# Optimization experiments

Measured on AMD Instinct MI355X. Metric: run time of the kernel, lower is better.

The kernel has to match this reference:

```python
import jax, jax.numpy as jnp
import numpy as np

B, SX, SY, D = 32, 2048, 2048, 160

def setup_inputs() -> dict:
    key = jax.random.key(0)
    ks = jax.random.split(key, 5)
    s = 1.0 / np.sqrt(D)
    return {
        "x": jax.random.normal(ks[0], (B, SX, D), dtype=jnp.float32),
        "y": jax.random.normal(ks[1], (B, SY, D), dtype=jnp.float32),
        "Wq": jax.random.normal(ks[2], (D, D), dtype=jnp.float32) * s,
        "bq": jnp.zeros((D,), dtype=jnp.float32),
        "Wk": jax.random.normal(ks[3], (D, D), dtype=jnp.float32) * s,
        "bk": jnp.zeros((D,), dtype=jnp.float32),
        "Wv": jax.random.normal(ks[4], (D, D), dtype=jnp.float32) * s,
        "bv": jnp.zeros((D,), dtype=jnp.float32),
    }

def reference(x, y, Wq, bq, Wk, bk, Wv, bv):
    # torch nn.Linear: out = in @ W.T + b, W is [out_dim, in_dim]
    q = jnp.einsum('bxd,ed->bxe', x, Wq) + bq          # [B,SX,D]
    k = jnp.einsum('byd,ed->bye', y, Wk) + bk          # [B,SY,D]
    v = jnp.einsum('byd,ed->bye', y, Wv) + bv          # [B,SY,D]
    scores = jnp.einsum('bxd,byd->bxy', q, k)          # [B,SX,SY] (no scaling in source)
    attn = jax.nn.softmax(scores, axis=-1)
    out = jnp.einsum('bxy,byd->bxd', attn, v)          # dropout is identity at eval
    return out + x                                     # residual
```

## Files before the change

kernel.cpp:

```cpp
#include <hip/hip_runtime.h>

#define LOG2E 1.44269504088896340736f

typedef _Float16 f16;
typedef __attribute__((ext_vector_type(2))) _Float16 f16x2;
typedef __attribute__((ext_vector_type(4))) _Float16 f16x4;
typedef __attribute__((ext_vector_type(8))) _Float16 f16x8;
typedef __attribute__((ext_vector_type(4))) float f32x4;
typedef __attribute__((ext_vector_type(16))) float f32x16;
typedef __attribute__((ext_vector_type(8))) unsigned short us8;

#define BB 32
#define SSX 2048
#define SSY 2048
#define DD 160
#define M_TOTAL (BB*SSX)

#define PRS 168
#define VTRS 136
#define RS 168

__device__ __forceinline__ f32x4 mfma16(f16x8 a, f16x8 b, f32x4 c) {
  return __builtin_amdgcn_mfma_f32_16x16x32_f16(a, b, c, 0, 0, 0);
}

__device__ __forceinline__ f32x16 mfma32(f16x8 a, f16x8 b, f32x16 c) {
  return __builtin_amdgcn_mfma_f32_32x32x16_f16(a, b, c, 0, 0, 0);
}

__device__ __forceinline__ unsigned pk2(float a, float b) {
  union { f16x2 h; unsigned u; } x;
  x.h = (f16x2){(f16)a, (f16)b};
  return x.u;
}

__global__ __launch_bounds__(256, 3) void proj_kernel(
    const float* __restrict__ x, const float* __restrict__ y,
    const float* __restrict__ Wq, const float* __restrict__ bq,
    const float* __restrict__ Wk, const float* __restrict__ bk,
    const float* __restrict__ Wv, const float* __restrict__ bv,
    f16* __restrict__ Qw, f16* __restrict__ Kw, f16* __restrict__ Vtw)
{
  __shared__ __align__(16) f16 buf[160*PRS];
  const int t = threadIdx.x;
  const int wave = t >> 6;
  const int lane = t & 63;
  const int quad = lane >> 4;
  const int l16  = lane & 15;
  const int bid  = (blockIdx.x & 7) * 192 + (blockIdx.x >> 3);
  const int kind = bid % 3;
  const int tile = bid / 3;
  const int row0 = tile * 128;
  const float* src  = (kind == 0) ? x  : y;
  const float* W    = (kind == 0) ? Wq : (kind == 1 ? Wk : Wv);
  const float* bias = (kind == 0) ? bq : (kind == 1 ? bk : bv);

  for (int i = 0; i < 20; ++i) {
    int idx = t + i*256;
    int r = idx / 40, c4 = idx % 40;
    float4 v = *(const float4*)&src[(size_t)(row0 + r)*DD + c4*4];
    f16x4 h = { (f16)v.x, (f16)v.y, (f16)v.z, (f16)v.w };
    *(f16x4*)&buf[r*PRS + c4*4] = h;
  }
  __syncthreads();
  f16x8 afr0[5], afr1[5];
  #pragma unroll
  for (int ks = 0; ks < 5; ++ks) {
    afr0[ks] = *(const f16x8*)&buf[(wave*32 + l16)*PRS + ks*32 + quad*8];
    afr1[ks] = *(const f16x8*)&buf[(wave*32 + 16 + l16)*PRS + ks*32 + quad*8];
  }
  __syncthreads();

  for (int i = 0; i < 25; ++i) {
    int idx = t + i*256;
    int r = idx / 40, c4 = idx % 40;
    float4 v = *(const float4*)&W[r*160 + c4*4];
    f16x4 h = { (f16)v.x, (f16)v.y, (f16)v.z, (f16)v.w };
    *(f16x4*)&buf[r*PRS + c4*4] = h;
  }
  __syncthreads();

  f32x4 acc0[10], acc1[10];
  #pragma unroll
  for (int nt = 0; nt < 10; ++nt) {
    float bs = bias[nt*16 + l16];
    acc0[nt] = (f32x4){bs,bs,bs,bs};
    acc1[nt] = (f32x4){bs,bs,bs,bs};
    #pragma unroll
    for (int ks = 0; ks < 5; ++ks) {
      f16x8 bfr = *(const f16x8*)&buf[(nt*16 + l16)*PRS + ks*32 + quad*8];
      acc0[nt] = mfma16(afr0[ks], bfr, acc0[nt]);
      acc1[nt] = mfma16(afr1[ks], bfr, acc1[nt]);
    }
  }
  __syncthreads();

  if (kind < 2) {
    f16* dst = (kind == 0) ? Qw : Kw;
    #pragma unroll
    for (int nt = 0; nt < 10; ++nt)
      #pragma unroll
      for (int r = 0; r < 4; ++r) {
        buf[(wave*32 + quad*4 + r)*PRS + nt*16 + l16]      = (f16)acc0[nt][r];
        buf[(wave*32 + 16 + quad*4 + r)*PRS + nt*16 + l16] = (f16)acc1[nt][r];
      }
    __syncthreads();
    for (int i = 0; i < 10; ++i) {
      int idx = t + i*256;
      int r = idx / 20, g = idx % 20;
      *(us8*)&dst[(size_t)(row0 + r)*DD + g*8] = *(const us8*)&buf[r*PRS + g*8];
    }
  } else {
    #pragma unroll
    for (int nt = 0; nt < 10; ++nt)
      #pragma unroll
      for (int r = 0; r < 4; ++r) {
        buf[(nt*16 + l16)*VTRS + wave*32 + quad*4 + r]      = (f16)acc0[nt][r];
        buf[(nt*16 + l16)*VTRS + wave*32 + 16 + quad*4 + r] = (f16)acc1[nt][r];
      }
    __syncthreads();
    const int b  = row0 / SSY;
    const int y0 = row0 % SSY;
    for (int i = 0; i < 10; ++i) {
      int idx = t + i*256;
      int d = idx / 16, yg = idx % 16;
      *(us8*)&Vtw[((size_t)b*DD + d)*SSY + y0 + yg*8] = *(const us8*)&buf[d*VTRS + yg*8];
    }
  }
}


#define LOAD_CHUNK(yb) { \
  const f16* ksrc = Kw + ((size_t)b*SSY + (yb))*DD; \
  const f16* vsrc = Vtw + (size_t)b*DD*SSY + (yb); \
  _Pragma("unroll") \
  for (int i = 0; i < 5; ++i) { \
    int idx = t + i*256; int r = idx/20, c = idx%20; \
    kreg[i] = *(const us8*)&ksrc[(size_t)r*DD + c*8]; \
  } \
  _Pragma("unroll") \
  for (int i = 0; i < 5; ++i) { \
    int idx = t + i*256; int d = idx>>3, g = idx&7; \
    vreg[i] = *(const us8*)&vsrc[(size_t)d*SSY + g*8]; \
  } \
}

#define STORE_CHUNK() { \
  _Pragma("unroll") \
  for (int i = 0; i < 5; ++i) { \
    int idx = t + i*256; int r = idx/20, c = idx%20; \
    *(us8*)&K_lds[r*RS + c*8] = kreg[i]; \
  } \
  _Pragma("unroll") \
  for (int i = 0; i < 5; ++i) { \
    int idx = t + i*256; int d = idx>>3, g = idx&7; \
    *(us8*)&Vt_lds[d*64 + ((g ^ (d & 7)) << 3)] = vreg[i]; \
  } \
}

__global__ __launch_bounds__(256, 2) void flash_kernel(
    const f16* __restrict__ Qw, const f16* __restrict__ Kw, const f16* __restrict__ Vtw,
    const float* __restrict__ x, float* __restrict__ out)
{
  __shared__ __align__(16) f16 K_lds[64*RS];
  __shared__ __align__(16) f16 Vt_lds[160*64];
  const int t = threadIdx.x;
  const int wave = t >> 6;
  const int lane = t & 63;
  const int l31  = lane & 31;
  const int hi   = lane >> 5;
  const int bid  = (blockIdx.x & 7) * 64 + (blockIdx.x >> 3);
  const int b    = bid >> 4;
  const int x0   = (bid & 15) * 128;

  us8 kreg[5], vreg[5];
  LOAD_CHUNK(0);

  f16x8 qfr[10];
  #pragma unroll
  for (int h = 0; h < 2; ++h) {
    if (h) __syncthreads();
    const f16* qsrc = Qw + ((size_t)b*SSX + x0 + h*64)*DD;
    for (int i = 0; i < 5; ++i) {
      int idx = t + i*256;
      int r = idx / 20, c = idx % 20;
      *(us8*)&K_lds[r*RS + c*8] = *(const us8*)&qsrc[(size_t)r*DD + c*8];
    }
    __syncthreads();
    if ((wave >> 1) == h) {
      const int base = (wave & 1)*32;
      #pragma unroll
      for (int s = 0; s < 10; ++s)
        qfr[s] = *(const f16x8*)&K_lds[(base + l31)*RS + s*16 + hi*8];
    }
  }

  f32x16 acc[5];
  #pragma unroll
  for (int i = 0; i < 5; ++i)
    #pragma unroll
    for (int r = 0; r < 16; ++r) acc[i][r] = 0.f;
  float m = -1e30f, l = 0.f;

  for (int yc = 0; yc < SSY/64; ++yc) {
    __syncthreads();
    STORE_CHUNK();
    __syncthreads();
    if (yc < SSY/64 - 1) LOAD_CHUNK((yc+1)*64);

    f32x16 S0, S1;
    #pragma unroll
    for (int r = 0; r < 16; ++r) { S0[r] = 0.f; S1[r] = 0.f; }
    __builtin_amdgcn_s_setprio(1);
    #pragma unroll
    for (int s = 0; s < 10; ++s) {
      f16x8 k0 = *(const f16x8*)&K_lds[l31*RS + s*16 + hi*8];
      f16x8 k1 = *(const f16x8*)&K_lds[(32 + l31)*RS + s*16 + hi*8];
      S0 = mfma32(k0, qfr[s], S0);
      S1 = mfma32(k1, qfr[s], S1);
    }
    __builtin_amdgcn_s_setprio(0);

    float pmax = fmaxf(S0[0], S0[1]);
    #pragma unroll
    for (int r = 2; r < 16; r += 2) pmax = fmaxf(pmax, fmaxf(S0[r], S0[r+1]));
    #pragma unroll
    for (int r = 0; r < 16; r += 2) pmax = fmaxf(pmax, fmaxf(S1[r], S1[r+1]));
    pmax = fmaxf(pmax, __shfl_xor(pmax, 32));

    if (__any(pmax > m + 8.f)) {
      float n  = fmaxf(m, pmax);
      float sc = exp2f((m - n)*LOG2E);
      m = n; l *= sc;
      #pragma unroll
      for (int r = 0; r < 16; ++r) {
        float scq = __shfl(sc, (r&3) + 8*(r>>2) + 4*hi);
        #pragma unroll
        for (int dt = 0; dt < 5; ++dt) acc[dt][r] *= scq;
      }
    }

    float lsum = 0.f;
    #pragma unroll
    for (int r = 0; r < 16; ++r) { S0[r] = exp2f((S0[r] - m)*LOG2E); lsum += S0[r]; }
    #pragma unroll
    for (int r = 0; r < 16; ++r) { S1[r] = exp2f((S1[r] - m)*LOG2E); lsum += S1[r]; }
    lsum += __shfl_xor(lsum, 32);
    l += lsum;

    #pragma unroll
    for (int c = 0; c < 4; ++c) {
      const int bo = (c & 1)*8;
      unsigned L0, L1, H0, H1;
      if (c < 2) {
        L0 = pk2(S0[bo+0], S0[bo+1]); L1 = pk2(S0[bo+2], S0[bo+3]);
        H0 = pk2(S0[bo+4], S0[bo+5]); H1 = pk2(S0[bo+6], S0[bo+7]);
      } else {
        L0 = pk2(S1[bo+0], S1[bo+1]); L1 = pk2(S1[bo+2], S1[bo+3]);
        H0 = pk2(S1[bo+4], S1[bo+5]); H1 = pk2(S1[bo+6], S1[bo+7]);
      }
      unsigned sd0 = hi ? L0 : H0;
      unsigned sd1 = hi ? L1 : H1;
      unsigned rc0 = (unsigned)__shfl_xor((int)sd0, 32);
      unsigned rc1 = (unsigned)__shfl_xor((int)sd1, 32);
      union { unsigned u[4]; f16x8 h; } pw;
      pw.u[0] = hi ? rc0 : L0;
      pw.u[1] = hi ? rc1 : L1;
      pw.u[2] = hi ? H0 : rc0;
      pw.u[3] = hi ? H1 : rc1;
      __builtin_amdgcn_s_setprio(1);
      #pragma unroll
      for (int dt = 0; dt < 5; ++dt) {
        int row = dt*32 + l31;
        f16x8 vf = *(const f16x8*)&Vt_lds[row*64 + (((c*2 + hi) ^ (row & 7)) << 3)];
        acc[dt] = mfma32(pw.h, vf, acc[dt]);
      }
      __builtin_amdgcn_s_setprio(0);
    }
  }

  #pragma unroll
  for (int r = 0; r < 16; ++r) {
    int qr = (r&3) + 8*(r>>2) + 4*hi;
    float rl = 1.f / __shfl(l, qr);
    size_t rowoff = ((size_t)b*SSX + x0 + wave*32 + qr)*DD + l31;
    #pragma unroll
    for (int dt = 0; dt < 5; ++dt) {
      size_t o = rowoff + (size_t)dt*32;
      out[o] = acc[dt][r]*rl + x[o];
    }
  }
}

extern "C" void kernel_launch(void* const* d_in, const int* in_sizes, int n_in,
                              void* d_out, int out_size, void* d_ws, size_t ws_size,
                              hipStream_t stream) {
  const float* x  = (const float*)d_in[0];
  const float* y  = (const float*)d_in[1];
  const float* Wq = (const float*)d_in[2];
  const float* bq = (const float*)d_in[3];
  const float* Wk = (const float*)d_in[4];
  const float* bk = (const float*)d_in[5];
  const float* Wv = (const float*)d_in[6];
  const float* bv = (const float*)d_in[7];

  f16* Qw  = (f16*)d_ws;
  f16* Kw  = Qw + (size_t)M_TOTAL*DD;
  f16* Vtw = Kw + (size_t)M_TOTAL*DD;

  proj_kernel<<<1536, 256, 0, stream>>>(x, y, Wq, bq, Wk, bk, Wv, bv, Qw, Kw, Vtw);
  flash_kernel<<<512, 256, 0, stream>>>(Qw, Kw, Vtw, x, (float*)d_out);
}
```

Measured before the change: 282.0 us.

## Read V fragments straight from global, double-buffer K in LDS, use permlane32 swap

V^T is no longer staged through LDS. Each wave loads its MFMA B-operand fragments for V directly from global memory into registers, split into two halves so the loads can overlap with the softmax work. K is double-buffered in LDS, which removes one of the two barriers per iteration. The P repacking now uses round-toward-zero pack conversion and permlane32_swap in place of two shuffles plus selects. The cost is more global and L2 traffic, because every wave reads the full V tile, plus higher register pressure from holding 20 V fragments, which risks occupancy and exposed global latency.

New measurement: 417.0 us. 47.9% more time.

```diff
diff --git a/kernel.cpp b/kernel.cpp
--- a/kernel.cpp
+++ b/kernel.cpp
@@ -4,11 +4,13 @@
 
 typedef _Float16 f16;
 typedef __attribute__((ext_vector_type(2))) _Float16 f16x2;
+typedef __attribute__((ext_vector_type(2))) __fp16 fp16x2;
 typedef __attribute__((ext_vector_type(4))) _Float16 f16x4;
 typedef __attribute__((ext_vector_type(8))) _Float16 f16x8;
 typedef __attribute__((ext_vector_type(4))) float f32x4;
 typedef __attribute__((ext_vector_type(16))) float f32x16;
 typedef __attribute__((ext_vector_type(8))) unsigned short us8;
+typedef __attribute__((ext_vector_type(2))) int i32x2;
 
 #define BB 32
 #define SSX 2048
@@ -28,9 +30,9 @@
   return __builtin_amdgcn_mfma_f32_32x32x16_f16(a, b, c, 0, 0, 0);
 }
 
-__device__ __forceinline__ unsigned pk2(float a, float b) {
-  union { f16x2 h; unsigned u; } x;
-  x.h = (f16x2){(f16)a, (f16)b};
+__device__ __forceinline__ unsigned pk2rtz(float a, float b) {
+  union { fp16x2 h; unsigned u; } x;
+  x.h = __builtin_amdgcn_cvt_pkrtz(a, b);
   return x.u;
 }
 
@@ -130,31 +132,20 @@
 }
 
 
-#define LOAD_CHUNK(yb) { \
+#define LOAD_K(yb) { \
   const f16* ksrc = Kw + ((size_t)b*SSY + (yb))*DD; \
-  const f16* vsrc = Vtw + (size_t)b*DD*SSY + (yb); \
   _Pragma("unroll") \
   for (int i = 0; i < 5; ++i) { \
     int idx = t + i*256; int r = idx/20, c = idx%20; \
     kreg[i] = *(const us8*)&ksrc[(size_t)r*DD + c*8]; \
   } \
-  _Pragma("unroll") \
-  for (int i = 0; i < 5; ++i) { \
-    int idx = t + i*256; int d = idx>>3, g = idx&7; \
-    vreg[i] = *(const us8*)&vsrc[(size_t)d*SSY + g*8]; \
-  } \
-}
-
-#define STORE_CHUNK() { \
+}
+
+#define STORE_K(cb) { \
   _Pragma("unroll") \
   for (int i = 0; i < 5; ++i) { \
     int idx = t + i*256; int r = idx/20, c = idx%20; \
-    *(us8*)&K_lds[r*RS + c*8] = kreg[i]; \
-  } \
-  _Pragma("unroll") \
-  for (int i = 0; i < 5; ++i) { \
-    int idx = t + i*256; int d = idx>>3, g = idx&7; \
-    *(us8*)&Vt_lds[d*64 + ((g ^ (d & 7)) << 3)] = vreg[i]; \
+    *(us8*)&K_lds[cb][r*RS + c*8] = kreg[i]; \
   } \
 }
 
@@ -162,8 +153,7 @@
     const f16* __restrict__ Qw, const f16* __restrict__ Kw, const f16* __restrict__ Vtw,
     const float* __restrict__ x, float* __restrict__ out)
 {
-  __shared__ __align__(16) f16 K_lds[64*RS];
-  __shared__ __align__(16) f16 Vt_lds[160*64];
+  __shared__ __align__(16) f16 K_lds[2][64*RS];
   const int t = threadIdx.x;
   const int wave = t >> 6;
   const int lane = t & 63;
@@ -173,27 +163,38 @@
   const int b    = bid >> 4;
   const int x0   = (bid & 15) * 128;
 
-  us8 kreg[5], vreg[5];
-  LOAD_CHUNK(0);
+  us8 kreg[5];
+  LOAD_K(0);
 
   f16x8 qfr[10];
-  #pragma unroll
-  for (int h = 0; h < 2; ++h) {
-    if (h) __syncthreads();
-    const f16* qsrc = Qw + ((size_t)b*SSX + x0 + h*64)*DD;
-    for (int i = 0; i < 5; ++i) {
-      int idx = t + i*256;
-      int r = idx / 20, c = idx % 20;
-      *(us8*)&K_lds[r*RS + c*8] = *(const us8*)&qsrc[(size_t)r*DD + c*8];
-    }
-    __syncthreads();
-    if ((wave >> 1) == h) {
-      const int base = (wave & 1)*32;
-      #pragma unroll
-      for (int s = 0; s < 10; ++s)
-        qfr[s] = *(const f16x8*)&K_lds[(base + l31)*RS + s*16 + hi*8];
-    }
-  }
+  const f16* qsrc = Qw + ((size_t)b*SSX + x0)*DD;
+  #pragma unroll
+  for (int i = 0; i < 5; ++i) {
+    int idx = t + i*256; int r = idx/20, c = idx%20;
+    *(us8*)&K_lds[0][r*RS + c*8] = *(const us8*)&qsrc[(size_t)r*DD + c*8];
+  }
+  __syncthreads();
+  if ((wave >> 1) == 0) {
+    const int base = (wave & 1)*32;
+    #pragma unroll
+    for (int s = 0; s < 10; ++s)
+      qfr[s] = *(const f16x8*)&K_lds[0][(base + l31)*RS + s*16 + hi*8];
+  }
+  #pragma unroll
+  for (int i = 0; i < 5; ++i) {
+    int idx = t + i*256; int r = idx/20, c = idx%20;
+    *(us8*)&K_lds[1][r*RS + c*8] = *(const us8*)&qsrc[(size_t)(64 + r)*DD + c*8];
+  }
+  __syncthreads();
+  if ((wave >> 1) == 1) {
+    const int base = (wave & 1)*32;
+    #pragma unroll
+    for (int s = 0; s < 10; ++s)
+      qfr[s] = *(const f16x8*)&K_lds[1][(base + l31)*RS + s*16 + hi*8];
+  }
+  STORE_K(0);
+  LOAD_K(64);
+  __syncthreads();
 
   f32x16 acc[5];
   #pragma unroll
@@ -202,11 +203,14 @@
     for (int r = 0; r < 16; ++r) acc[i][r] = 0.f;
   float m = -1e30f, l = 0.f;
 
+  const f16* vp0 = Vtw + (size_t)b*DD*SSY + (size_t)l31*SSY + hi*8;
+  const f16* vp1 = vp0 + (size_t)32*SSY;
+  const f16* vp2 = vp0 + (size_t)64*SSY;
+  const f16* vp3 = vp0 + (size_t)96*SSY;
+  const f16* vp4 = vp0 + (size_t)128*SSY;
+
   for (int yc = 0; yc < SSY/64; ++yc) {
-    __syncthreads();
-    STORE_CHUNK();
-    __syncthreads();
-    if (yc < SSY/64 - 1) LOAD_CHUNK((yc+1)*64);
+    const int cur = yc & 1;
 
     f32x16 S0, S1;
     #pragma unroll
@@ -214,18 +218,31 @@
     __builtin_amdgcn_s_setprio(1);
     #pragma unroll
     for (int s = 0; s < 10; ++s) {
-      f16x8 k0 = *(const f16x8*)&K_lds[l31*RS + s*16 + hi*8];
-      f16x8 k1 = *(const f16x8*)&K_lds[(32 + l31)*RS + s*16 + hi*8];
+      f16x8 k0 = *(const f16x8*)&K_lds[cur][l31*RS + s*16 + hi*8];
+      f16x8 k1 = *(const f16x8*)&K_lds[cur][(32 + l31)*RS + s*16 + hi*8];
       S0 = mfma32(k0, qfr[s], S0);
       S1 = mfma32(k1, qfr[s], S1);
     }
     __builtin_amdgcn_s_setprio(0);
 
+    f16x8 vf[4][5];
+    #pragma unroll
+    for (int c = 0; c < 2; ++c) {
+      vf[c][0] = *(const f16x8*)&vp0[c*16];
+      vf[c][1] = *(const f16x8*)&vp1[c*16];
+      vf[c][2] = *(const f16x8*)&vp2[c*16];
+      vf[c][3] = *(const f16x8*)&vp3[c*16];
+      vf[c][4] = *(const f16x8*)&vp4[c*16];
+    }
+
+    if (yc < SSY/64 - 1) STORE_K(cur ^ 1);
+    if (yc < SSY/64 - 2) LOAD_K((yc+2)*64);
+
     float pmax = fmaxf(S0[0], S0[1]);
     #pragma unroll
-    for (int r = 2; r < 16; r += 2) pmax = fmaxf(pmax, fmaxf(S0[r], S0[r+1]));
-    #pragma unroll
-    for (int r = 0; r < 16; r += 2) pmax = fmaxf(pmax, fmaxf(S1[r], S1[r+1]));
+    for (int r = 2; r < 16; r += 2) pmax = fmaxf(fmaxf(pmax, S0[r]), S0[r+1]);
+    #pragma unroll
+    for (int r = 0; r < 16; r += 2) pmax = fmaxf(fmaxf(pmax, S1[r]), S1[r+1]);
     pmax = fmaxf(pmax, __shfl_xor(pmax, 32));
 
     if (__any(pmax > m + 8.f)) {
@@ -249,34 +266,47 @@
     l += lsum;
 
     #pragma unroll
+    for (int c = 2; c < 4; ++c) {
+      vf[c][0] = *(const f16x8*)&vp0[c*16];
+      vf[c][1] = *(const f16x8*)&vp1[c*16];
+      vf[c][2] = *(const f16x8*)&vp2[c*16];
+      vf[c][3] = *(const f16x8*)&vp3[c*16];
+      vf[c][4] = *(const f16x8*)&vp4[c*16];
+    }
+
+    unsigned pw[4][4];
+    #pragma unroll
     for (int c = 0; c < 4; ++c) {
       const int bo = (c & 1)*8;
-      unsigned L0, L1, H0, H1;
-      if (c < 2) {
-        L0 = pk2(S0[bo+0], S0[bo+1]); L1 = pk2(S0[bo+2], S0[bo+3]);
-        H0 = pk2(S0[bo+4], S0[bo+5]); H1 = pk2(S0[bo+6], S0[bo+7]);
-      } else {
-        L0 = pk2(S1[bo+0], S1[bo+1]); L1 = pk2(S1[bo+2], S1[bo+3]);
-        H0 = pk2(S1[bo+4], S1[bo+5]); H1 = pk2(S1[bo+6], S1[bo+7]);
-      }
-      unsigned sd0 = hi ? L0 : H0;
-      unsigned sd1 = hi ? L1 : H1;
-      unsigned rc0 = (unsigned)__shfl_xor((int)sd0, 32);
-      unsigned rc1 = (unsigned)__shfl_xor((int)sd1, 32);
-      union { unsigned u[4]; f16x8 h; } pw;
-      pw.u[0] = hi ? rc0 : L0;
-      pw.u[1] = hi ? rc1 : L1;
-      pw.u[2] = hi ? H0 : rc0;
-      pw.u[3] = hi ? H1 : rc1;
-      __builtin_amdgcn_s_setprio(1);
+      float s0 = (c < 2) ? S0[bo+0] : S1[bo+0];
+      float s1 = (c < 2) ? S0[bo+1] : S1[bo+1];
+      float s2 = (c < 2) ? S0[bo+2] : S1[bo+2];
+      float s3 = (c < 2) ? S0[bo+3] : S1[bo+3];
+      float s4 = (c < 2) ? S0[bo+4] : S1[bo+4];
+      float s5 = (c < 2) ? S0[bo+5] : S1[bo+5];
+      float s6 = (c < 2) ? S0[bo+6] : S1[bo+6];
+      float s7 = (c < 2) ? S0[bo+7] : S1[bo+7];
+      unsigned L0 = pk2rtz(s0, s1), L1 = pk2rtz(s2, s3);
+      unsigned H0 = pk2rtz(s4, s5), H1 = pk2rtz(s6, s7);
+      i32x2 r02 = __builtin_amdgcn_permlane32_swap((int)L0, (int)H0, false, false);
+      i32x2 r13 = __builtin_amdgcn_permlane32_swap((int)L1, (int)H1, false, false);
+      pw[c][0] = (unsigned)r02.x; pw[c][1] = (unsigned)r13.x;
+      pw[c][2] = (unsigned)r02.y; pw[c][3] = (unsigned)r13.y;
+    }
+
+    __builtin_amdgcn_s_setprio(1);
+    #pragma unroll
+    for (int c = 0; c < 4; ++c) {
+      union { unsigned u[4]; f16x8 h; } ph;
+      ph.u[0] = pw[c][0]; ph.u[1] = pw[c][1]; ph.u[2] = pw[c][2]; ph.u[3] = pw[c][3];
       #pragma unroll
-      for (int dt = 0; dt < 5; ++dt) {
-        int row = dt*32 + l31;
-        f16x8 vf = *(const f16x8*)&Vt_lds[row*64 + (((c*2 + hi) ^ (row & 7)) << 3)];
-        acc[dt] = mfma32(pw.h, vf, acc[dt]);
-      }
-      __builtin_amdgcn_s_setprio(0);
-    }
+      for (int dt = 0; dt < 5; ++dt)
+        acc[dt] = mfma32(ph.h, vf[c][dt], acc[dt]);
+    }
+    __builtin_amdgcn_s_setprio(0);
+
+    vp0 += 64; vp1 += 64; vp2 += 64; vp3 += 64; vp4 += 64;
+    __syncthreads();
   }
 
   #pragma unroll
```
